# Kernel tuning notes

Hardware: AMD Instinct MI355X
Metric: run time of the kernel (lower is better)

Reference implementation:

```python
import jax, jax.numpy as jnp
import numpy as np

N_NODES = 50000
N_EDGES = 800000
IN_DIM = 512
HID_DIM = 128


def setup_inputs() -> dict:
    key = jax.random.key(0)
    k1, k2, k3 = jax.random.split(key, 3)
    x = jax.random.normal(k1, (N_NODES, IN_DIM), dtype=jnp.float32)
    edge_index = jax.random.randint(k2, (2, N_EDGES), 0, N_NODES, dtype=jnp.int32)
    # GCNConv weight (glorot-ish scale) and bias
    W = jax.random.normal(k3, (IN_DIM, HID_DIM), dtype=jnp.float32) * (1.0 / np.sqrt(IN_DIM))
    b = jnp.zeros((HID_DIM,), dtype=jnp.float32)
    # PReLU per-channel slope, torch default init 0.25
    prelu_w = jnp.full((HID_DIM,), 0.25, dtype=jnp.float32)
    return {"x": x, "edge_index": edge_index, "W": W, "b": b, "prelu_w": prelu_w}


def reference(x, edge_index, W, b, prelu_w):
    N = x.shape[0]
    # 1) linear transform first (GCNConv transforms then aggregates)
    h = x @ W  # [N, H]
    # 2) add self-loops
    loop = jnp.arange(N, dtype=edge_index.dtype)
    src = jnp.concatenate([edge_index[0], loop])  # [E+N]
    dst = jnp.concatenate([edge_index[1], loop])  # [E+N]
    # 3) symmetric degree normalization deg^-1/2 (self-loops guarantee deg>=1)
    deg = jax.ops.segment_sum(jnp.ones_like(dst, dtype=h.dtype), dst, num_segments=N)
    dinv = jax.lax.rsqrt(deg)
    norm = dinv[src] * dinv[dst]  # [E+N]
    # 4) gather-scale-scatter aggregation
    msg = h[src] * norm[:, None]  # [E+N, H]
    out = jax.ops.segment_sum(msg, dst, num_segments=N) + b  # [N, H]
    # 5) per-channel PReLU
    return jnp.where(out > 0, out, prelu_w * out)
```

## Files before the change

kernel.cpp:

```cpp
#include <hip/hip_runtime.h>

#define IN_DIM 512
#define HID 128
#define BK 64

#define RANGE 98
#define BCAP  2048
#define CSTR  32

typedef float f4 __attribute__((ext_vector_type(4)));
typedef short bf8 __attribute__((ext_vector_type(8)));

__device__ inline unsigned short f2bf(float f) {
    unsigned u = __float_as_uint(f);
    unsigned r = (u + 0x7FFFu + ((u >> 16) & 1u)) >> 16;
    return (unsigned short)r;
}
__device__ inline float bf2f(unsigned short u) {
    return __uint_as_float(((unsigned)u) << 16);
}

__global__ __launch_bounds__(256) void k_bin(const int* __restrict__ src,
                                             const int* __restrict__ dst,
                                             int* __restrict__ bcnt,
                                             int2* __restrict__ buckets, int E) {
    int e0 = (blockIdx.x * 256 + threadIdx.x) * 4;
    if (e0 >= E) return;
    if (e0 + 4 <= E) {
        int4 s4 = *(const int4*)(src + e0);
        int4 d4 = *(const int4*)(dst + e0);
        int ss[4] = {s4.x, s4.y, s4.z, s4.w};
        int dd[4] = {d4.x, d4.y, d4.z, d4.w};
#pragma unroll
        for (int i = 0; i < 4; i++) {
            int b = dd[i] / RANGE;
            int pos = atomicAdd(&bcnt[b * CSTR], 1);
            if (pos < BCAP) buckets[(size_t)b * BCAP + pos] = make_int2(ss[i], dd[i]);
        }
    } else {
        for (int e = e0; e < E; e++) {
            int d = dst[e];
            int b = d / RANGE;
            int pos = atomicAdd(&bcnt[b * CSTR], 1);
            if (pos < BCAP) buckets[(size_t)b * BCAP + pos] = make_int2(src[e], d);
        }
    }
}

__global__ __launch_bounds__(512) void k_bscan(const int* __restrict__ bcnt,
                                               int* __restrict__ bbase, int NB,
                                               int* __restrict__ rowStart,
                                               int N, int E) {
    __shared__ int s[512];
    int t = threadIdx.x;
    int v = (t < NB) ? min(bcnt[t * CSTR], BCAP) : 0;
    s[t] = v;
    __syncthreads();
    for (int off = 1; off < 512; off <<= 1) {
        int y = (t >= off) ? s[t - off] : 0;
        __syncthreads();
        s[t] += y;
        __syncthreads();
    }
    if (t < NB) bbase[t] = s[t] - v;
    if (t == 0) rowStart[N] = E;
}

__global__ __launch_bounds__(256) void k_binfill(const int2* __restrict__ buckets,
                                                 const int* __restrict__ bcnt,
                                                 const int* __restrict__ bbase,
                                                 int* __restrict__ rowStart,
                                                 float* __restrict__ dinv,
                                                 int* __restrict__ esrc, int N) {
    __shared__ int bins[RANGE];
    __shared__ int cur[RANGE];
    __shared__ int ss[128];
    __shared__ int seg[BCAP];
    const int b = blockIdx.x;
    const int t = threadIdx.x;
    const int cnt = min(bcnt[b * CSTR], BCAP);
    const int base = bbase[b];
    const int n0 = b * RANGE;
    const int2* bp = buckets + (size_t)b * BCAP;

    for (int i = t; i < RANGE; i += 256) bins[i] = 0;
    __syncthreads();
    for (int i = t; i < cnt; i += 256) atomicAdd(&bins[bp[i].y - n0], 1);
    __syncthreads();
    int v = (t < RANGE) ? bins[t] : 0;
    if (t < 128) ss[t] = v;
    __syncthreads();
    for (int off = 1; off < 128; off <<= 1) {
        int y = (t >= off && t < 128) ? ss[t - off] : 0;
        __syncthreads();
        if (t < 128) ss[t] += y;
        __syncthreads();
    }
    if (t < RANGE) {
        int ex = ss[t] - v;
        cur[t] = ex;
        int g = n0 + t;
        if (g < N) {
            rowStart[g] = base + ex;
            dinv[g] = rsqrtf((float)(v + 1));
        }
    }
    __syncthreads();
    for (int i = t; i < cnt; i += 256) {
        int2 p = bp[i];
        int r = atomicAdd(&cur[p.y - n0], 1);
        seg[r] = p.x;
    }
    __syncthreads();
    for (int i = t; i < cnt; i += 256) esrc[base + i] = seg[i];
}

__global__ __launch_bounds__(256) void k_convW(const float* __restrict__ W,
                                               unsigned short* __restrict__ Wt) {
    int id = blockIdx.x * 256 + threadIdx.x;
    int n = id & (HID - 1);
    int k = id >> 7;
    Wt[(size_t)n * IN_DIM + k] = f2bf(W[(size_t)k * HID + n]);
}

__global__ __launch_bounds__(256, 2) void k_gemm(const float* __restrict__ x,
                                                 const unsigned short* __restrict__ Wt,
                                                 unsigned short* __restrict__ h, int M) {
    __shared__ unsigned short As[128][BK + 8];
    __shared__ unsigned short Bs[128][BK + 8];
    const int t = threadIdx.x;
    const int wave = t >> 6, lane = t & 63;
    const int row0 = blockIdx.x * 128;
    const int quad = lane >> 4, l16 = lane & 15;

    f4 acc[2][8];
#pragma unroll
    for (int i = 0; i < 2; i++)
#pragma unroll
        for (int j = 0; j < 8; j++) acc[i][j] = (f4){0.f, 0.f, 0.f, 0.f};

    const int srow = t >> 1;
    const int shalf = t & 1;
    const bool rowok = (row0 + srow) < M;
    const float* xrow = x + (size_t)(row0 + srow) * IN_DIM + shalf * 32;
    const unsigned short* wrow = Wt + (size_t)srow * IN_DIM + shalf * 32;

    for (int k0 = 0; k0 < IN_DIM; k0 += BK) {
        float4 v[8];
#pragma unroll
        for (int i = 0; i < 8; i++)
            v[i] = rowok ? *(const float4*)(xrow + k0 + i * 4)
                         : make_float4(0.f, 0.f, 0.f, 0.f);
        unsigned short tmp[32];
#pragma unroll
        for (int i = 0; i < 8; i++) {
            tmp[i * 4 + 0] = f2bf(v[i].x);
            tmp[i * 4 + 1] = f2bf(v[i].y);
            tmp[i * 4 + 2] = f2bf(v[i].z);
            tmp[i * 4 + 3] = f2bf(v[i].w);
        }
#pragma unroll
        for (int i = 0; i < 4; i++)
            *(float4*)&As[srow][shalf * 32 + i * 8] = *(float4*)&tmp[i * 8];
#pragma unroll
        for (int i = 0; i < 4; i++)
            *(float4*)&Bs[srow][shalf * 32 + i * 8] =
                *(const float4*)(wrow + k0 + i * 8);
        __syncthreads();

#pragma unroll
        for (int ks = 0; ks < BK; ks += 32) {
            bf8 af[2];
#pragma unroll
            for (int rt = 0; rt < 2; rt++)
                af[rt] = *(const bf8*)&As[wave * 32 + rt * 16 + l16][ks + quad * 8];
#pragma unroll
            for (int nt = 0; nt < 8; nt++) {
                bf8 bfv = *(const bf8*)&Bs[nt * 16 + l16][ks + quad * 8];
#pragma unroll
                for (int rt = 0; rt < 2; rt++)
                    acc[rt][nt] = __builtin_amdgcn_mfma_f32_16x16x32_bf16(
                        af[rt], bfv, acc[rt][nt], 0, 0, 0);
            }
        }
        __syncthreads();
    }

#pragma unroll
    for (int rt = 0; rt < 2; rt++) {
#pragma unroll
        for (int reg = 0; reg < 4; reg++) {
            int row = row0 + wave * 32 + rt * 16 + quad * 4 + reg;
            if (row < M) {
#pragma unroll
                for (int nt = 0; nt < 8; nt++) {
                    int col = nt * 16 + l16;
                    h[(size_t)row * HID + col] = f2bf(acc[rt][nt][reg]);
                }
            }
        }
    }
}

__global__ __launch_bounds__(256) void k_pull(const unsigned short* __restrict__ h,
                                              const int* __restrict__ esrc,
                                              const int* __restrict__ rowStart,
                                              const float* __restrict__ dinv,
                                              const float* __restrict__ bias,
                                              const float* __restrict__ pw,
                                              float* __restrict__ out, int N) {
    int gid = blockIdx.x * 256 + threadIdx.x;
    int node = gid >> 5;
    int l = threadIdx.x & 31;
    if (node >= N) return;
    int e0 = rowStart[node], e1 = rowStart[node + 1];
    float di = dinv[node];
    const int ci = l * 4;
    ushort4 hv = *(const ushort4*)&h[(size_t)node * HID + ci];
    float s2 = di * di;
    float ax = bf2f(hv.x) * s2, ay = bf2f(hv.y) * s2;
    float az = bf2f(hv.z) * s2, aw = bf2f(hv.w) * s2;
    int j = e0;
    for (; j + 4 <= e1; j += 4) {
        int s0 = esrc[j], s1 = esrc[j + 1], s2i = esrc[j + 2], s3 = esrc[j + 3];
        float w0 = dinv[s0] * di, w1 = dinv[s1] * di;
        float w2 = dinv[s2i] * di, w3 = dinv[s3] * di;
        ushort4 a0 = *(const ushort4*)&h[(size_t)s0 * HID + ci];
        ushort4 a1 = *(const ushort4*)&h[(size_t)s1 * HID + ci];
        ushort4 a2 = *(const ushort4*)&h[(size_t)s2i * HID + ci];
        ushort4 a3 = *(const ushort4*)&h[(size_t)s3 * HID + ci];
        ax += bf2f(a0.x) * w0 + bf2f(a1.x) * w1 + bf2f(a2.x) * w2 + bf2f(a3.x) * w3;
        ay += bf2f(a0.y) * w0 + bf2f(a1.y) * w1 + bf2f(a2.y) * w2 + bf2f(a3.y) * w3;
        az += bf2f(a0.z) * w0 + bf2f(a1.z) * w1 + bf2f(a2.z) * w2 + bf2f(a3.z) * w3;
        aw += bf2f(a0.w) * w0 + bf2f(a1.w) * w1 + bf2f(a2.w) * w2 + bf2f(a3.w) * w3;
    }
    for (; j < e1; j++) {
        int s = esrc[j];
        float w = dinv[s] * di;
        ushort4 a = *(const ushort4*)&h[(size_t)s * HID + ci];
        ax += bf2f(a.x) * w; ay += bf2f(a.y) * w;
        az += bf2f(a.z) * w; aw += bf2f(a.w) * w;
    }
    float4 bv = *(const float4*)&bias[ci];
    float4 pv = *(const float4*)&pw[ci];
    float ox = ax + bv.x, oy = ay + bv.y, oz = az + bv.z, ow = aw + bv.w;
    ox = ox > 0.f ? ox : pv.x * ox;
    oy = oy > 0.f ? oy : pv.y * oy;
    oz = oz > 0.f ? oz : pv.z * oz;
    ow = ow > 0.f ? ow : pv.w * ow;
    *(float4*)&out[(size_t)node * HID + ci] = make_float4(ox, oy, oz, ow);
}

extern "C" void kernel_launch(void* const* d_in, const int* in_sizes, int n_in,
                              void* d_out, int out_size, void* d_ws, size_t ws_size,
                              hipStream_t stream) {
    const float* x  = (const float*)d_in[0];
    const int*   ei = (const int*)d_in[1];
    const float* W  = (const float*)d_in[2];
    const float* b  = (const float*)d_in[3];
    const float* pw = (const float*)d_in[4];

    const int N = in_sizes[0] / IN_DIM;
    const int E = in_sizes[1] / 2;
    const int* src = ei;
    const int* dst = ei + E;

    const int NB = (N + RANGE - 1) / RANGE;

    char* ws = (char*)d_ws;
    size_t off = 0;
    auto carve = [&](size_t bytes) -> void* {
        void* p = ws + off;
        off = (off + bytes + 255) & ~(size_t)255;
        return p;
    };
    unsigned short* h = (unsigned short*)carve((size_t)N * HID * sizeof(unsigned short));
    int*   rowStart = (int*)carve((size_t)(N + 1) * sizeof(int));
    float* dinv     = (float*)carve((size_t)N * sizeof(float));
    int*   esrc     = (int*)carve((size_t)E * sizeof(int));
    unsigned short* Wt = (unsigned short*)carve((size_t)IN_DIM * HID * sizeof(unsigned short));
    int*   bcnt     = (int*)carve((size_t)NB * CSTR * sizeof(int));
    int*   bbase    = (int*)carve((size_t)NB * sizeof(int));
    int2*  buckets  = (int2*)carve((size_t)NB * BCAP * sizeof(int2));

    hipMemsetAsync(bcnt, 0, (size_t)NB * CSTR * sizeof(int), stream);

    k_convW<<<(IN_DIM * HID) / 256, 256, 0, stream>>>(W, Wt);
    k_gemm<<<(N + 127) / 128, 256, 0, stream>>>(x, Wt, h, N);
    k_bin<<<(E / 4 + 255) / 256, 256, 0, stream>>>(src, dst, bcnt, buckets, E);
    k_bscan<<<1, 512, 0, stream>>>(bcnt, bbase, NB, rowStart, N, E);
    k_binfill<<<NB, 256, 0, stream>>>(buckets, bcnt, bbase, rowStart, dinv, esrc, N);
    k_pull<<<(int)(((size_t)N * 32 + 255) / 256), 256, 0, stream>>>(
        h, esrc, rowStart, dinv, b, pw, (float*)d_out, N);
}
```

Measured before the change: 263.3 us.

## Split edge bucket counters into 8 groups and pack edges into single ints

Edge binning now spreads atomics across 8 per-block-group counter arrays and sub-buckets instead of one padded counter per bucket, to cut contention on the hot global atomics. Each edge is packed into one 32-bit word (local destination in the high 7 bits, source in the low 25), which halves bucket traffic compared with int2 pairs. The fill kernel walks the 8 sub-buckets per bin. Capacities are per sub-bucket, so a skewed distribution could overflow and drop edges, and the 25-bit source field limits node count.

```diff
diff --git a/kernel.cpp b/kernel.cpp
--- a/kernel.cpp
+++ b/kernel.cpp
@@ -5,8 +5,10 @@
 #define BK 64
 
 #define RANGE 98
-#define BCAP  2048
-#define CSTR  32
+#define NGRP 8
+#define NBPAD 512
+#define SUBCAP 384
+#define BCAP 2560
 
 typedef float f4 __attribute__((ext_vector_type(4)));
 typedef short bf8 __attribute__((ext_vector_type(8)));
@@ -23,7 +25,11 @@
 __global__ __launch_bounds__(256) void k_bin(const int* __restrict__ src,
                                              const int* __restrict__ dst,
                                              int* __restrict__ bcnt,
-                                             int2* __restrict__ buckets, int E) {
+                                             int* __restrict__ buckets,
+                                             int E, int NB) {
+    const int grp = blockIdx.x & (NGRP - 1);
+    int* gcnt = bcnt + grp * NBPAD;
+    int* gbuck = buckets + (size_t)grp * NB * SUBCAP;
     int e0 = (blockIdx.x * 256 + threadIdx.x) * 4;
     if (e0 >= E) return;
     if (e0 + 4 <= E) {
@@ -34,26 +40,32 @@
 #pragma unroll
         for (int i = 0; i < 4; i++) {
             int b = dd[i] / RANGE;
-            int pos = atomicAdd(&bcnt[b * CSTR], 1);
-            if (pos < BCAP) buckets[(size_t)b * BCAP + pos] = make_int2(ss[i], dd[i]);
+            int ld = dd[i] - b * RANGE;
+            int pos = atomicAdd(&gcnt[b], 1);
+            if (pos < SUBCAP) gbuck[b * SUBCAP + pos] = (ld << 25) | ss[i];
         }
     } else {
         for (int e = e0; e < E; e++) {
             int d = dst[e];
             int b = d / RANGE;
-            int pos = atomicAdd(&bcnt[b * CSTR], 1);
-            if (pos < BCAP) buckets[(size_t)b * BCAP + pos] = make_int2(src[e], d);
+            int ld = d - b * RANGE;
+            int pos = atomicAdd(&gcnt[b], 1);
+            if (pos < SUBCAP) gbuck[b * SUBCAP + pos] = (ld << 25) | src[e];
         }
     }
 }
 
 __global__ __launch_bounds__(512) void k_bscan(const int* __restrict__ bcnt,
                                                int* __restrict__ bbase, int NB,
-                                               int* __restrict__ rowStart,
-                                               int N, int E) {
+                                               int* __restrict__ rowStart, int N) {
     __shared__ int s[512];
     int t = threadIdx.x;
-    int v = (t < NB) ? min(bcnt[t * CSTR], BCAP) : 0;
+    int v = 0;
+    if (t < NB) {
+#pragma unroll
+        for (int g = 0; g < NGRP; g++) v += min(bcnt[g * NBPAD + t], SUBCAP);
+        v = min(v, BCAP);
+    }
     s[t] = v;
     __syncthreads();
     for (int off = 1; off < 512; off <<= 1) {
@@ -63,29 +75,42 @@
         __syncthreads();
     }
     if (t < NB) bbase[t] = s[t] - v;
-    if (t == 0) rowStart[N] = E;
-}
-
-__global__ __launch_bounds__(256) void k_binfill(const int2* __restrict__ buckets,
+    if (t == NB - 1) rowStart[N] = s[t];
+}
+
+__global__ __launch_bounds__(256) void k_binfill(const int* __restrict__ buckets,
                                                  const int* __restrict__ bcnt,
                                                  const int* __restrict__ bbase,
                                                  int* __restrict__ rowStart,
                                                  float* __restrict__ dinv,
-                                                 int* __restrict__ esrc, int N) {
+                                                 int* __restrict__ esrc,
+                                                 int N, int NB) {
     __shared__ int bins[RANGE];
     __shared__ int cur[RANGE];
     __shared__ int ss[128];
     __shared__ int seg[BCAP];
     const int b = blockIdx.x;
     const int t = threadIdx.x;
-    const int cnt = min(bcnt[b * CSTR], BCAP);
     const int base = bbase[b];
     const int n0 = b * RANGE;
-    const int2* bp = buckets + (size_t)b * BCAP;
+
+    int scnt[NGRP];
+    int total = 0;
+#pragma unroll
+    for (int g = 0; g < NGRP; g++) {
+        scnt[g] = min(bcnt[g * NBPAD + b], SUBCAP);
+        total += scnt[g];
+    }
+    total = min(total, BCAP);
 
     for (int i = t; i < RANGE; i += 256) bins[i] = 0;
     __syncthreads();
-    for (int i = t; i < cnt; i += 256) atomicAdd(&bins[bp[i].y - n0], 1);
+#pragma unroll
+    for (int g = 0; g < NGRP; g++) {
+        const int* sb = buckets + ((size_t)g * NB + b) * SUBCAP;
+        for (int i = t; i < scnt[g]; i += 256)
+            atomicAdd(&bins[((unsigned)sb[i]) >> 25], 1);
+    }
     __syncthreads();
     int v = (t < RANGE) ? bins[t] : 0;
     if (t < 128) ss[t] = v;
@@ -106,13 +131,17 @@
         }
     }
     __syncthreads();
-    for (int i = t; i < cnt; i += 256) {
-        int2 p = bp[i];
-        int r = atomicAdd(&cur[p.y - n0], 1);
-        seg[r] = p.x;
-    }
-    __syncthreads();
-    for (int i = t; i < cnt; i += 256) esrc[base + i] = seg[i];
+#pragma unroll
+    for (int g = 0; g < NGRP; g++) {
+        const int* sb = buckets + ((size_t)g * NB + b) * SUBCAP;
+        for (int i = t; i < scnt[g]; i += 256) {
+            int w = sb[i];
+            int r = atomicAdd(&cur[((unsigned)w) >> 25], 1);
+            if (r < BCAP) seg[r] = w & 0x1FFFFFF;
+        }
+    }
+    __syncthreads();
+    for (int i = t; i < total; i += 256) esrc[base + i] = seg[i];
 }
 
 __global__ __launch_bounds__(256) void k_convW(const float* __restrict__ W,
@@ -279,17 +308,17 @@
     float* dinv     = (float*)carve((size_t)N * sizeof(float));
     int*   esrc     = (int*)carve((size_t)E * sizeof(int));
     unsigned short* Wt = (unsigned short*)carve((size_t)IN_DIM * HID * sizeof(unsigned short));
-    int*   bcnt     = (int*)carve((size_t)NB * CSTR * sizeof(int));
+    int*   bcnt     = (int*)carve((size_t)NGRP * NBPAD * sizeof(int));
     int*   bbase    = (int*)carve((size_t)NB * sizeof(int));
-    int2*  buckets  = (int2*)carve((size_t)NB * BCAP * sizeof(int2));
-
-    hipMemsetAsync(bcnt, 0, (size_t)NB * CSTR * sizeof(int), stream);
+    int*   buckets  = (int*)carve((size_t)NGRP * NB * SUBCAP * sizeof(int));
+
+    hipMemsetAsync(bcnt, 0, (size_t)NGRP * NBPAD * sizeof(int), stream);
 
     k_convW<<<(IN_DIM * HID) / 256, 256, 0, stream>>>(W, Wt);
     k_gemm<<<(N + 127) / 128, 256, 0, stream>>>(x, Wt, h, N);
-    k_bin<<<(E / 4 + 255) / 256, 256, 0, stream>>>(src, dst, bcnt, buckets, E);
-    k_bscan<<<1, 512, 0, stream>>>(bcnt, bbase, NB, rowStart, N, E);
-    k_binfill<<<NB, 256, 0, stream>>>(buckets, bcnt, bbase, rowStart, dinv, esrc, N);
+    k_bin<<<(E / 4 + 255) / 256, 256, 0, stream>>>(src, dst, bcnt, buckets, E, NB);
+    k_bscan<<<1, 512, 0, stream>>>(bcnt, bbase, NB, rowStart, N);
+    k_binfill<<<NB, 256, 0, stream>>>(buckets, bcnt, bbase, rowStart, dinv, esrc, N, NB);
     k_pull<<<(int)(((size_t)N * 32 + 255) / 256), 256, 0, stream>>>(
         h, esrc, rowStart, dinv, b, pw, (float*)d_out, N);
 }
```

Result: no change. 262.8 us (-0.2%).

## Replace global-atomic bucketing with two-pass block-local counting sort into packed buffer

Applied to the files above, without the earlier changes.

Edge binning no longer uses global atomics into fixed-capacity buckets. A per-block LDS histogram pass, a column scan over a bins-by-blocks count matrix and a total scan now give exact offsets. A scatter pass then writes packed 32-bit (local dst, src) words into a dense buffer. This removes global atomic contention, the memset and the 8-byte padded buckets, at the cost of two extra small kernels, a second read of the edge arrays, and hard-coded NB_/NBLK constants tied to the problem size.

```diff
diff --git a/kernel.cpp b/kernel.cpp
--- a/kernel.cpp
+++ b/kernel.cpp
@@ -5,8 +5,9 @@
 #define BK 64
 
 #define RANGE 98
-#define BCAP  2048
-#define CSTR  32
+#define NB_ 511
+#define NBLK 200
+#define SEGCAP 2048
 
 typedef float f4 __attribute__((ext_vector_type(4)));
 typedef short bf8 __attribute__((ext_vector_type(8)));
@@ -19,41 +20,60 @@
 __device__ inline float bf2f(unsigned short u) {
     return __uint_as_float(((unsigned)u) << 16);
 }
-
-__global__ __launch_bounds__(256) void k_bin(const int* __restrict__ src,
-                                             const int* __restrict__ dst,
-                                             int* __restrict__ bcnt,
-                                             int2* __restrict__ buckets, int E) {
-    int e0 = (blockIdx.x * 256 + threadIdx.x) * 4;
-    if (e0 >= E) return;
-    if (e0 + 4 <= E) {
-        int4 s4 = *(const int4*)(src + e0);
-        int4 d4 = *(const int4*)(dst + e0);
-        int ss[4] = {s4.x, s4.y, s4.z, s4.w};
-        int dd[4] = {d4.x, d4.y, d4.z, d4.w};
-#pragma unroll
-        for (int i = 0; i < 4; i++) {
-            int b = dd[i] / RANGE;
-            int pos = atomicAdd(&bcnt[b * CSTR], 1);
-            if (pos < BCAP) buckets[(size_t)b * BCAP + pos] = make_int2(ss[i], dd[i]);
-        }
-    } else {
-        for (int e = e0; e < E; e++) {
-            int d = dst[e];
-            int b = d / RANGE;
-            int pos = atomicAdd(&bcnt[b * CSTR], 1);
-            if (pos < BCAP) buckets[(size_t)b * BCAP + pos] = make_int2(src[e], d);
-        }
-    }
-}
-
-__global__ __launch_bounds__(512) void k_bscan(const int* __restrict__ bcnt,
-                                               int* __restrict__ bbase, int NB,
+__device__ inline int xcd_perm(int blk) {
+    return (blk & 7) * (NBLK / 8) + (blk >> 3);
+}
+
+__global__ __launch_bounds__(256) void k_count(const int* __restrict__ dst,
+                                               int* __restrict__ cmat, int E) {
+    __shared__ int bins[NB_];
+    const int blk = blockIdx.x, t = threadIdx.x;
+    const int chunk = (((E + NBLK - 1) / NBLK) + 3) & ~3;
+    const int start = blk * chunk;
+    const int end = min(E, start + chunk);
+    for (int i = t; i < NB_; i += 256) bins[i] = 0;
+    __syncthreads();
+    if (start < E) {
+        int nvec = (end - start) >> 2;
+        for (int i = t; i < nvec; i += 256) {
+            int4 d4 = *(const int4*)(dst + start + i * 4);
+            atomicAdd(&bins[d4.x / RANGE], 1);
+            atomicAdd(&bins[d4.y / RANGE], 1);
+            atomicAdd(&bins[d4.z / RANGE], 1);
+            atomicAdd(&bins[d4.w / RANGE], 1);
+        }
+        for (int i = start + nvec * 4 + t; i < end; i += 256)
+            atomicAdd(&bins[dst[i] / RANGE], 1);
+    }
+    __syncthreads();
+    const int p = xcd_perm(blk);
+    for (int j = t; j < NB_; j += 256) cmat[j * NBLK + p] = bins[j];
+}
+
+__global__ __launch_bounds__(256) void k_cscan(int* __restrict__ cmat,
+                                               int* __restrict__ tot) {
+    __shared__ int s[256];
+    const int j = blockIdx.x, t = threadIdx.x;
+    int v = (t < NBLK) ? cmat[j * NBLK + t] : 0;
+    s[t] = v;
+    __syncthreads();
+    for (int off = 1; off < 256; off <<= 1) {
+        int y = (t >= off) ? s[t - off] : 0;
+        __syncthreads();
+        s[t] += y;
+        __syncthreads();
+    }
+    if (t < NBLK) cmat[j * NBLK + t] = s[t] - v;
+    if (t == 255) tot[j] = s[255];
+}
+
+__global__ __launch_bounds__(512) void k_tscan(const int* __restrict__ tot,
+                                               int* __restrict__ bbase,
                                                int* __restrict__ rowStart,
                                                int N, int E) {
     __shared__ int s[512];
     int t = threadIdx.x;
-    int v = (t < NB) ? min(bcnt[t * CSTR], BCAP) : 0;
+    int v = (t < NB_) ? tot[t] : 0;
     s[t] = v;
     __syncthreads();
     for (int off = 1; off < 512; off <<= 1) {
@@ -62,12 +82,49 @@
         s[t] += y;
         __syncthreads();
     }
-    if (t < NB) bbase[t] = s[t] - v;
+    if (t < NB_) bbase[t] = s[t] - v;
     if (t == 0) rowStart[N] = E;
 }
 
-__global__ __launch_bounds__(256) void k_binfill(const int2* __restrict__ buckets,
-                                                 const int* __restrict__ bcnt,
+__global__ __launch_bounds__(256) void k_scatter(const int* __restrict__ src,
+                                                 const int* __restrict__ dst,
+                                                 const int* __restrict__ cmat,
+                                                 const int* __restrict__ bbase,
+                                                 unsigned* __restrict__ ebuf, int E) {
+    __shared__ int cur[NB_];
+    const int blk = blockIdx.x, t = threadIdx.x;
+    const int p = xcd_perm(blk);
+    for (int j = t; j < NB_; j += 256) cur[j] = bbase[j] + cmat[j * NBLK + p];
+    __syncthreads();
+    const int chunk = (((E + NBLK - 1) / NBLK) + 3) & ~3;
+    const int start = blk * chunk;
+    const int end = min(E, start + chunk);
+    if (start >= E) return;
+    int nvec = (end - start) >> 2;
+    for (int i = t; i < nvec; i += 256) {
+        int4 s4 = *(const int4*)(src + start + i * 4);
+        int4 d4 = *(const int4*)(dst + start + i * 4);
+        int ss[4] = {s4.x, s4.y, s4.z, s4.w};
+        int dd[4] = {d4.x, d4.y, d4.z, d4.w};
+#pragma unroll
+        for (int k = 0; k < 4; k++) {
+            int b = dd[k] / RANGE;
+            int ld = dd[k] - b * RANGE;
+            int pos = atomicAdd(&cur[b], 1);
+            ebuf[pos] = ((unsigned)ld << 25) | (unsigned)ss[k];
+        }
+    }
+    for (int i = start + nvec * 4 + t; i < end; i += 256) {
+        int d = dst[i];
+        int b = d / RANGE;
+        int ld = d - b * RANGE;
+        int pos = atomicAdd(&cur[b], 1);
+        ebuf[pos] = ((unsigned)ld << 25) | (unsigned)src[i];
+    }
+}
+
+__global__ __launch_bounds__(256) void k_binfill(const unsigned* __restrict__ ebuf,
+                                                 const int* __restrict__ tot,
                                                  const int* __restrict__ bbase,
                                                  int* __restrict__ rowStart,
                                                  float* __restrict__ dinv,
@@ -75,17 +132,17 @@
     __shared__ int bins[RANGE];
     __shared__ int cur[RANGE];
     __shared__ int ss[128];
-    __shared__ int seg[BCAP];
+    __shared__ int seg[SEGCAP];
     const int b = blockIdx.x;
     const int t = threadIdx.x;
-    const int cnt = min(bcnt[b * CSTR], BCAP);
     const int base = bbase[b];
+    const int cnt = min(tot[b], SEGCAP);
     const int n0 = b * RANGE;
-    const int2* bp = buckets + (size_t)b * BCAP;
+    const unsigned* ep = ebuf + base;
 
     for (int i = t; i < RANGE; i += 256) bins[i] = 0;
     __syncthreads();
-    for (int i = t; i < cnt; i += 256) atomicAdd(&bins[bp[i].y - n0], 1);
+    for (int i = t; i < cnt; i += 256) atomicAdd(&bins[ep[i] >> 25], 1);
     __syncthreads();
     int v = (t < RANGE) ? bins[t] : 0;
     if (t < 128) ss[t] = v;
@@ -107,9 +164,9 @@
     }
     __syncthreads();
     for (int i = t; i < cnt; i += 256) {
-        int2 p = bp[i];
-        int r = atomicAdd(&cur[p.y - n0], 1);
-        seg[r] = p.x;
+        unsigned w = ep[i];
+        int r = atomicAdd(&cur[w >> 25], 1);
+        if (r < SEGCAP) seg[r] = (int)(w & 0x1FFFFFFu);
     }
     __syncthreads();
     for (int i = t; i < cnt; i += 256) esrc[base + i] = seg[i];
@@ -265,8 +322,6 @@
     const int* src = ei;
     const int* dst = ei + E;
 
-    const int NB = (N + RANGE - 1) / RANGE;
-
     char* ws = (char*)d_ws;
     size_t off = 0;
     auto carve = [&](size_t bytes) -> void* {
@@ -279,17 +334,18 @@
     float* dinv     = (float*)carve((size_t)N * sizeof(float));
     int*   esrc     = (int*)carve((size_t)E * sizeof(int));
     unsigned short* Wt = (unsigned short*)carve((size_t)IN_DIM * HID * sizeof(unsigned short));
-    int*   bcnt     = (int*)carve((size_t)NB * CSTR * sizeof(int));
-    int*   bbase    = (int*)carve((size_t)NB * sizeof(int));
-    int2*  buckets  = (int2*)carve((size_t)NB * BCAP * sizeof(int2));
-
-    hipMemsetAsync(bcnt, 0, (size_t)NB * CSTR * sizeof(int), stream);
+    int*   cmat     = (int*)carve((size_t)NB_ * NBLK * sizeof(int));
+    int*   tot      = (int*)carve((size_t)NB_ * sizeof(int));
+    int*   bbase    = (int*)carve((size_t)NB_ * sizeof(int));
+    unsigned* ebuf  = (unsigned*)carve((size_t)E * sizeof(unsigned));
 
     k_convW<<<(IN_DIM * HID) / 256, 256, 0, stream>>>(W, Wt);
     k_gemm<<<(N + 127) / 128, 256, 0, stream>>>(x, Wt, h, N);
-    k_bin<<<(E / 4 + 255) / 256, 256, 0, stream>>>(src, dst, bcnt, buckets, E);
-    k_bscan<<<1, 512, 0, stream>>>(bcnt, bbase, NB, rowStart, N, E);
-    k_binfill<<<NB, 256, 0, stream>>>(buckets, bcnt, bbase, rowStart, dinv, esrc, N);
+    k_count<<<NBLK, 256, 0, stream>>>(dst, cmat, E);
+    k_cscan<<<NB_, 256, 0, stream>>>(cmat, tot);
+    k_tscan<<<1, 512, 0, stream>>>(tot, bbase, rowStart, N, E);
+    k_scatter<<<NBLK, 256, 0, stream>>>(src, dst, cmat, bbase, ebuf, E);
+    k_binfill<<<NB_, 256, 0, stream>>>(ebuf, tot, bbase, rowStart, dinv, esrc, N);
     k_pull<<<(int)(((size_t)N * 32 + 255) / 256), 256, 0, stream>>>(
         h, esrc, rowStart, dinv, b, pw, (float*)d_out, N);
 }
```

Result: faster. 239.1 us (-9.2%).
